# Optimization experiments

Measured on AMD Instinct MI355X. Metric: run time of the kernel, lower is better.

Reference implementation:

```python
import jax, jax.numpy as jnp
import numpy as np

N_HEAD = 16
NEG_BIG = 1e10  # matches the torch module's -10000000000.0 additive mask


def setup_inputs() -> dict:
    key = jax.random.key(0)
    k1, k2, k3 = jax.random.split(key, 3)
    B, T, D = 2, 2048, 1024
    x = jax.random.normal(k1, (B, T, D), dtype=jnp.float32)
    W_attn = jax.random.normal(k2, (D, 3 * D), dtype=jnp.float32) * 0.02
    b_attn = jnp.zeros((3 * D,), dtype=jnp.float32)
    W_proj = jax.random.normal(k3, (D, D), dtype=jnp.float32) * 0.02
    b_proj = jnp.zeros((D,), dtype=jnp.float32)
    return {"x": x, "W_attn": W_attn, "b_attn": b_attn,
            "W_proj": W_proj, "b_proj": b_proj}


def reference(x, W_attn, b_attn, W_proj, b_proj):
    B, T, D = x.shape
    H = N_HEAD
    dh = D // H
    # c_attn: fused qkv projection
    qkv = x @ W_attn + b_attn                      # [B, T, 3D]
    q, k, v = jnp.split(qkv, 3, axis=-1)
    # split heads -> [B, H, T, dh]
    q = q.reshape(B, T, H, dh).transpose(0, 2, 1, 3)
    k = k.reshape(B, T, H, dh).transpose(0, 2, 1, 3)
    v = v.reshape(B, T, H, dh).transpose(0, 2, 1, 3)
    # scores [B, H, T, T]
    w = jnp.einsum("bhqd,bhkd->bhqk", q, k)
    w = w / jnp.sqrt(jnp.float32(dh))              # scale=True
    # causal additive mask: w*b - 1e10*(1-b), b = lower-triangular ones
    bias = jnp.tril(jnp.ones((T, T), dtype=w.dtype))
    w = w * bias - NEG_BIG * (1.0 - bias)
    w = jax.nn.softmax(w, axis=-1)
    a = jnp.einsum("bhqk,bhkd->bhqd", w, v)        # [B, H, T, dh]
    # merge heads
    a = a.transpose(0, 2, 1, 3).reshape(B, T, D)
    # c_proj
    return a @ W_proj + b_proj
```

## Files before the change

kernel.cpp:

```cpp
#include <hip/hip_runtime.h>
#include <hip/hip_bf16.h>


typedef unsigned short u16;
typedef unsigned int u32;
typedef __attribute__((ext_vector_type(4))) float f32x4;
typedef __attribute__((ext_vector_type(16))) float f32x16;
typedef __attribute__((ext_vector_type(8))) short bf16x8;
typedef __attribute__((ext_vector_type(4))) int i32x4;

__device__ __forceinline__ u16 f2bf(float f) {
  unsigned u = __builtin_bit_cast(unsigned, f);
  u += 0x7FFFu + ((u >> 16) & 1u);
  return (u16)(u >> 16);
}

__device__ __forceinline__ u32 cvtpk(float lo, float hi) {
  u32 r;
  asm("v_cvt_pk_bf16_f32 %0, %1, %2" : "=v"(r) : "v"(lo), "v"(hi));
  return r;
}

__device__ __forceinline__ void gl_lds16(const u16* g, u16* l) {
  __builtin_amdgcn_global_load_lds(
      (const __attribute__((address_space(1))) void*)g,
      (__attribute__((address_space(3))) void*)l, 16, 0, 0);
}

__global__ __launch_bounds__(256) void cast_bf16_kernel(const float* __restrict__ in,
                                                        u16* __restrict__ out, int n4) {
  int i = blockIdx.x * 256 + threadIdx.x;
  if (i < n4) {
    float4 f = reinterpret_cast<const float4*>(in)[i];
    ushort4 o;
    o.x = f2bf(f.x); o.y = f2bf(f.y); o.z = f2bf(f.z); o.w = f2bf(f.w);
    reinterpret_cast<ushort4*>(out)[i] = o;
  }
}

__global__ __launch_bounds__(256) void transpose_cast(const float* __restrict__ in,
                                                      u16* __restrict__ out, int R, int C) {
  __shared__ float tile[32][33];
  const int c0 = blockIdx.x * 32, r0 = blockIdx.y * 32;
  const int tx = threadIdx.x, ty = threadIdx.y;
#pragma unroll
  for (int i = 0; i < 4; ++i)
    tile[ty + 8 * i][tx] = in[(size_t)(r0 + ty + 8 * i) * C + c0 + tx];
  __syncthreads();
#pragma unroll
  for (int i = 0; i < 4; ++i)
    out[(size_t)(c0 + ty + 8 * i) * R + r0 + tx] = f2bf(tile[tx][ty + 8 * i]);
}

__global__ __launch_bounds__(256) void gemm_qkv(
    const u16* __restrict__ A, const u16* __restrict__ Bt, const float* __restrict__ bias,
    u16* __restrict__ Qh, u16* __restrict__ Kh, u16* __restrict__ Vh, int K) {
  __shared__ u16 As[128 * 32];
  __shared__ u16 Bs[128 * 32];
  const int tid = threadIdx.x;
  const int wave = tid >> 6, lane = tid & 63;
  const int kg = lane >> 4, rr = lane & 15;
  const int wm = wave >> 1, wn = wave & 1;
  const int nwg = gridDim.x * gridDim.y;
  const int lin = blockIdx.y * gridDim.x + blockIdx.x;
  const int swz = (lin & 7) * (nwg >> 3) + (lin >> 3);
  const int bx = swz % gridDim.x, by = swz / gridDim.x;
  const int rowA0 = by * 128, colB0 = bx * 128;

  const f32x4 z4 = {0.f, 0.f, 0.f, 0.f};
  f32x4 acc[4][4];
#pragma unroll
  for (int i = 0; i < 4; ++i)
#pragma unroll
    for (int j = 0; j < 4; ++j) acc[i][j] = z4;

  const int r_st = tid >> 2;
  const int c_st = (tid & 3) * 8;

  for (int k0 = 0; k0 < K; k0 += 32) {
#pragma unroll
    for (int i = 0; i < 2; ++i) {
      gl_lds16(A + (size_t)(rowA0 + i * 64 + r_st) * K + k0 + c_st,
               As + (i * 256 + (wave << 6)) * 8);
      gl_lds16(Bt + (size_t)(colB0 + i * 64 + r_st) * K + k0 + c_st,
               Bs + (i * 256 + (wave << 6)) * 8);
    }
    __syncthreads();

    bf16x8 af[4], bfr[4];
#pragma unroll
    for (int mi = 0; mi < 4; ++mi)
      af[mi] = *reinterpret_cast<const bf16x8*>(&As[(wm * 64 + mi * 16 + rr) * 32 + kg * 8]);
#pragma unroll
    for (int ni = 0; ni < 4; ++ni)
      bfr[ni] = *reinterpret_cast<const bf16x8*>(&Bs[(wn * 64 + ni * 16 + rr) * 32 + kg * 8]);
#pragma unroll
    for (int mi = 0; mi < 4; ++mi)
#pragma unroll
      for (int ni = 0; ni < 4; ++ni)
        acc[mi][ni] = __builtin_amdgcn_mfma_f32_16x16x32_bf16(af[mi], bfr[ni], acc[mi][ni], 0, 0, 0);
    __syncthreads();
  }

  const float QS = 0.125f * 1.44269504088896f;
#pragma unroll
  for (int mi = 0; mi < 4; ++mi) {
#pragma unroll
    for (int ni = 0; ni < 4; ++ni) {
      const int col = colB0 + wn * 64 + ni * 16 + rr;
      const float bcol = bias[col];
      f32x4 a = acc[mi][ni];
#pragma unroll
      for (int v = 0; v < 4; ++v) {
        const int row = rowA0 + wm * 64 + mi * 16 + kg * 4 + v;
        const float val = a[v] + bcol;
        const int b = row >> 11, t = row & 2047;
        const int which = col >> 10, d = col & 1023;
        const int h = d >> 6, dd = d & 63;
        const size_t idx = (((size_t)(b * 16 + h)) * 2048 + t) * 64 + dd;
        if (which == 0)
          Qh[idx] = f2bf(val * QS);
        else if (which == 1)
          Kh[idx] = f2bf(val);
        else
          Vh[idx] = f2bf(val);
      }
    }
  }
}

__global__ __launch_bounds__(256) void gemm_proj(
    const u16* __restrict__ A, const u16* __restrict__ Bt, const float* __restrict__ bias,
    float* __restrict__ outF, int N, int K) {
  __shared__ u16 As[128 * 32];
  __shared__ u16 Bs[64 * 32];
  const int tid = threadIdx.x;
  const int wave = tid >> 6, lane = tid & 63;
  const int kg = lane >> 4, rr = lane & 15;
  const int nwg = gridDim.x * gridDim.y;
  const int lin = blockIdx.y * gridDim.x + blockIdx.x;
  const int swz = (lin & 7) * (nwg >> 3) + (lin >> 3);
  const int bx = swz % gridDim.x, by = swz / gridDim.x;
  const int rowA0 = by * 128, colB0 = bx * 64;

  const f32x4 z4 = {0.f, 0.f, 0.f, 0.f};
  f32x4 acc[2][4];
#pragma unroll
  for (int i = 0; i < 2; ++i)
#pragma unroll
    for (int j = 0; j < 4; ++j) acc[i][j] = z4;

  const int r_st = tid >> 2;
  const int c_st = (tid & 3) * 8;

  for (int k0 = 0; k0 < K; k0 += 32) {
#pragma unroll
    for (int i = 0; i < 2; ++i)
      gl_lds16(A + (size_t)(rowA0 + i * 64 + r_st) * K + k0 + c_st,
               As + (i * 256 + (wave << 6)) * 8);
    gl_lds16(Bt + (size_t)(colB0 + r_st) * K + k0 + c_st, Bs + (wave << 6) * 8);
    __syncthreads();

    bf16x8 af[2], bfr[4];
#pragma unroll
    for (int mi = 0; mi < 2; ++mi)
      af[mi] = *reinterpret_cast<const bf16x8*>(&As[(wave * 32 + mi * 16 + rr) * 32 + kg * 8]);
#pragma unroll
    for (int ni = 0; ni < 4; ++ni)
      bfr[ni] = *reinterpret_cast<const bf16x8*>(&Bs[(ni * 16 + rr) * 32 + kg * 8]);
#pragma unroll
    for (int mi = 0; mi < 2; ++mi)
#pragma unroll
      for (int ni = 0; ni < 4; ++ni)
        acc[mi][ni] = __builtin_amdgcn_mfma_f32_16x16x32_bf16(af[mi], bfr[ni], acc[mi][ni], 0, 0, 0);
    __syncthreads();
  }

#pragma unroll
  for (int mi = 0; mi < 2; ++mi) {
#pragma unroll
    for (int ni = 0; ni < 4; ++ni) {
      const int col = colB0 + ni * 16 + rr;
      const float bcol = bias[col];
      f32x4 a = acc[mi][ni];
#pragma unroll
      for (int v = 0; v < 4; ++v) {
        const int row = rowA0 + wave * 32 + mi * 16 + kg * 4 + v;
        outF[(size_t)row * N + col] = a[v] + bcol;
      }
    }
  }
}

__global__ __launch_bounds__(256) void transpose_v(const u16* __restrict__ Vh,
                                                   u16* __restrict__ VhT) {
  __shared__ u16 tile[64][72];
  const int tid = threadIdx.x;
  const int t0 = blockIdx.x * 64;
  const int bh = blockIdx.y;
  const u16* src = Vh + ((size_t)bh * 2048 + t0) * 64;
  {
    const int ty = tid >> 2, tx = (tid & 3) * 16;
    *reinterpret_cast<bf16x8*>(&tile[ty][tx]) =
        *reinterpret_cast<const bf16x8*>(src + ty * 64 + tx);
    *reinterpret_cast<bf16x8*>(&tile[ty][tx + 8]) =
        *reinterpret_cast<const bf16x8*>(src + ty * 64 + tx + 8);
  }
  __syncthreads();
  {
    const int dd = tid >> 2, toff = (tid & 3) * 16;
    bf16x8 v0, v1;
#pragma unroll
    for (int j = 0; j < 8; ++j) v0[j] = (short)tile[toff + j][dd];
#pragma unroll
    for (int j = 0; j < 8; ++j) v1[j] = (short)tile[toff + 8 + j][dd];
    u16* dst = VhT + ((size_t)bh * 64 + dd) * 2048 + t0 + toff;
    *reinterpret_cast<bf16x8*>(dst) = v0;
    *reinterpret_cast<bf16x8*>(dst + 8) = v1;
  }
}

__device__ __forceinline__ void load_k(const u16* kptr, bf16x8 (&kA)[4], bf16x8 (&kB)[4]) {
#pragma unroll
  for (int ks = 0; ks < 4; ++ks) {
    kA[ks] = *reinterpret_cast<const bf16x8*>(kptr + ks * 16);
    kB[ks] = *reinterpret_cast<const bf16x8*>(kptr + 2048 + ks * 16);
  }
}

__device__ __forceinline__ void attn_step(
    int kvb, int n64, int myq, int hi, const u16* vbase,
    const bf16x8 (&qf)[4], const bf16x8 (&kA)[4], const bf16x8 (&kB)[4],
    f32x16& oA, f32x16& oB, float& m, float& l) {
  bf16x8 vfA[4], vfB[4];
  const u16* vp = vbase + kvb * 64;
#pragma unroll
  for (int ks = 0; ks < 4; ++ks) {
    vfA[ks] = *reinterpret_cast<const bf16x8*>(vp + ks * 16);
    vfB[ks] = *reinterpret_cast<const bf16x8*>(vp + 32 * 2048 + ks * 16);
  }

  f32x16 sA, sB;
#pragma unroll
  for (int i = 0; i < 16; ++i) { sA[i] = 0.f; sB[i] = 0.f; }
  __builtin_amdgcn_s_setprio(1);
#pragma unroll
  for (int ks = 0; ks < 4; ++ks)
    sA = __builtin_amdgcn_mfma_f32_32x32x16_bf16(kA[ks], qf[ks], sA, 0, 0, 0);
#pragma unroll
  for (int ks = 0; ks < 4; ++ks)
    sB = __builtin_amdgcn_mfma_f32_32x32x16_bf16(kB[ks], qf[ks], sB, 0, 0, 0);
  __builtin_amdgcn_s_setprio(0);

  if (kvb == n64 - 1) {
    const int kv0 = kvb * 64;
#pragma unroll
    for (int r = 0; r < 16; ++r) {
      const int kvA = kv0 + (r & 3) + 8 * (r >> 2) + 4 * hi;
      if (kvA > myq) sA[r] = -1e30f;
      if (kvA + 32 > myq) sB[r] = -1e30f;
    }
  }

  float pmax = -1e30f;
#pragma unroll
  for (int r = 0; r < 16; ++r) pmax = fmaxf(pmax, fmaxf(sA[r], sB[r]));
  pmax = fmaxf(pmax, __shfl_xor(pmax, 32));
  if (!__all(pmax - m <= 8.0f)) {
    const float mn = fmaxf(m, pmax);
    const float sc = __builtin_amdgcn_exp2f(m - mn);
    l *= sc;
    oA *= sc;
    oB *= sc;
    m = mn;
  }
  float rsum = 0.f;
#pragma unroll
  for (int r = 0; r < 16; ++r) {
    const float pa = __builtin_amdgcn_exp2f(sA[r] - m);
    const float pb = __builtin_amdgcn_exp2f(sB[r] - m);
    sA[r] = pa; sB[r] = pb;
    rsum += pa + pb;
  }
  rsum += __shfl_xor(rsum, 32);
  l += rsum;

  u32 pkA[8], pkB[8];
#pragma unroll
  for (int i = 0; i < 8; ++i) {
    pkA[i] = cvtpk(sA[2 * i], sA[2 * i + 1]);
    pkB[i] = cvtpk(sB[2 * i], sB[2 * i + 1]);
  }
  bf16x8 pf[4];
  {
    auto w0 = __builtin_amdgcn_permlane32_swap(pkA[0], pkA[2], false, false);
    auto w1 = __builtin_amdgcn_permlane32_swap(pkA[1], pkA[3], false, false);
    i32x4 t0 = {(int)w0[0], (int)w1[0], (int)w0[1], (int)w1[1]};
    pf[0] = __builtin_bit_cast(bf16x8, t0);
    auto w2 = __builtin_amdgcn_permlane32_swap(pkA[4], pkA[6], false, false);
    auto w3 = __builtin_amdgcn_permlane32_swap(pkA[5], pkA[7], false, false);
    i32x4 t1 = {(int)w2[0], (int)w3[0], (int)w2[1], (int)w3[1]};
    pf[1] = __builtin_bit_cast(bf16x8, t1);
    auto w4 = __builtin_amdgcn_permlane32_swap(pkB[0], pkB[2], false, false);
    auto w5 = __builtin_amdgcn_permlane32_swap(pkB[1], pkB[3], false, false);
    i32x4 t2 = {(int)w4[0], (int)w5[0], (int)w4[1], (int)w5[1]};
    pf[2] = __builtin_bit_cast(bf16x8, t2);
    auto w6 = __builtin_amdgcn_permlane32_swap(pkB[4], pkB[6], false, false);
    auto w7 = __builtin_amdgcn_permlane32_swap(pkB[5], pkB[7], false, false);
    i32x4 t3 = {(int)w6[0], (int)w7[0], (int)w6[1], (int)w7[1]};
    pf[3] = __builtin_bit_cast(bf16x8, t3);
  }

  __builtin_amdgcn_s_setprio(1);
#pragma unroll
  for (int ks = 0; ks < 4; ++ks)
    oA = __builtin_amdgcn_mfma_f32_32x32x16_bf16(vfA[ks], pf[ks], oA, 0, 0, 0);
#pragma unroll
  for (int ks = 0; ks < 4; ++ks)
    oB = __builtin_amdgcn_mfma_f32_32x32x16_bf16(vfB[ks], pf[ks], oB, 0, 0, 0);
  __builtin_amdgcn_s_setprio(0);
}

__global__ __launch_bounds__(256, 2) void attn_fwd(const u16* __restrict__ Qh,
                                                   const u16* __restrict__ Kh,
                                                   const u16* __restrict__ VhT,
                                                   u16* __restrict__ Ab) {
  __shared__ u16 Olq[4][32][80];
  __shared__ float Ml[4][2][32];
  const int tid = threadIdx.x;
  const int wave = tid >> 6, lane = tid & 63;
  const int lq = lane & 31, hi = lane >> 5;
  const int blk = blockIdx.x;
  const int qi = blk >> 5;
  const int bh = blk & 31;
  const int qtile = 63 - qi;
  const int q0 = qtile * 32;
  const int myq = q0 + lq;
  const size_t kvbase = (size_t)bh * 2048;

  const int n64 = (q0 + 32 + 63) >> 6;
  const int base = n64 >> 2, rem = n64 & 3;
  const int cnt = base + (wave < rem ? 1 : 0);
  const int start = wave * base + (wave < rem ? wave : rem);
  const int end = start + cnt;

  bf16x8 qf[4];
  {
    const u16* qptr = Qh + (kvbase + q0 + lq) * 64 + hi * 8;
#pragma unroll
    for (int ks = 0; ks < 4; ++ks)
      qf[ks] = *reinterpret_cast<const bf16x8*>(qptr + ks * 16);
  }

  f32x16 oA, oB;
#pragma unroll
  for (int i = 0; i < 16; ++i) { oA[i] = 0.f; oB[i] = 0.f; }
  float m = -1e30f, l = 0.f;

  const u16* kbase = Kh + (kvbase + lq) * 64 + hi * 8;
  const u16* vbase = VhT + ((size_t)bh * 64 + lq) * 2048 + hi * 8;

  bf16x8 kA0[4], kB0[4], kA1[4], kB1[4];
  int kvb = start;
  if (kvb < end) {
    load_k(kbase + (size_t)kvb * 4096, kA0, kB0);
    while (true) {
      if (kvb + 1 < end) load_k(kbase + (size_t)(kvb + 1) * 4096, kA1, kB1);
      attn_step(kvb, n64, myq, hi, vbase, qf, kA0, kB0, oA, oB, m, l);
      if (++kvb >= end) break;
      if (kvb + 1 < end) load_k(kbase + (size_t)(kvb + 1) * 4096, kA0, kB0);
      attn_step(kvb, n64, myq, hi, vbase, qf, kA1, kB1, oA, oB, m, l);
      if (++kvb >= end) break;
    }
  }

  if (hi == 0) {
    Ml[wave][0][lq] = m;
    Ml[wave][1][lq] = l;
  }
  {
    u32* orow = reinterpret_cast<u32*>(&Olq[wave][lq][0]);
#pragma unroll
    for (int qd = 0; qd < 4; ++qd) {
      const int dh0 = 8 * qd + 4 * hi;
      orow[(dh0 >> 1) + 0] = cvtpk(oA[4 * qd + 0], oA[4 * qd + 1]);
      orow[(dh0 >> 1) + 1] = cvtpk(oA[4 * qd + 2], oA[4 * qd + 3]);
      orow[((dh0 + 32) >> 1) + 0] = cvtpk(oB[4 * qd + 0], oB[4 * qd + 1]);
      orow[((dh0 + 32) >> 1) + 1] = cvtpk(oB[4 * qd + 2], oB[4 * qd + 3]);
    }
  }
  __syncthreads();

  const int col = tid >> 3;
  const int dh0 = (tid & 7) * 8;
  float M = -1e30f;
  float mw[4];
#pragma unroll
  for (int w = 0; w < 4; ++w) { mw[w] = Ml[w][0][col]; M = fmaxf(M, mw[w]); }
  float lsum = 0.f;
  float scw[4];
#pragma unroll
  for (int w = 0; w < 4; ++w) {
    scw[w] = __builtin_amdgcn_exp2f(mw[w] - M);
    lsum += scw[w] * Ml[w][1][col];
  }
  const float inv = 1.0f / lsum;
  float acc8[8];
#pragma unroll
  for (int i = 0; i < 8; ++i) acc8[i] = 0.f;
#pragma unroll
  for (int w = 0; w < 4; ++w) {
    bf16x8 ov = *reinterpret_cast<const bf16x8*>(&Olq[w][col][dh0]);
#pragma unroll
    for (int i = 0; i < 8; ++i) {
      const float f = __builtin_bit_cast(float, ((u32)(u16)ov[i]) << 16);
      acc8[i] += scw[w] * f;
    }
  }
  const int b = bh >> 4, h = bh & 15;
  bf16x8 outv;
#pragma unroll
  for (int i = 0; i < 8; ++i) outv[i] = (short)f2bf(acc8[i] * inv);
  *reinterpret_cast<bf16x8*>(Ab + ((size_t)b * 2048 + q0 + col) * 1024 + h * 64 + dh0) = outv;
}

extern "C" void kernel_launch(void* const* d_in, const int* in_sizes, int n_in,
                              void* d_out, int out_size, void* d_ws, size_t ws_size,
                              hipStream_t stream) {
  const float* x      = (const float*)d_in[0];
  const float* W_attn = (const float*)d_in[1];
  const float* b_attn = (const float*)d_in[2];
  const float* W_proj = (const float*)d_in[3];
  const float* b_proj = (const float*)d_in[4];
  float* out = (float*)d_out;

  u16* xb  = (u16*)d_ws;
  u16* Wat = xb + (size_t)4096 * 1024;
  u16* Wpt = Wat + (size_t)3072 * 1024;
  u16* Qh  = Wpt + (size_t)1024 * 1024;
  u16* Kh  = Qh + (size_t)4194304;
  u16* VhT = Kh + (size_t)4194304;
  u16* Ab  = VhT + (size_t)4194304;
  u16* Vh  = Ab;

  cast_bf16_kernel<<<4096, 256, 0, stream>>>(x, xb, 4096 * 1024 / 4);
  transpose_cast<<<dim3(96, 32), dim3(32, 8), 0, stream>>>(W_attn, Wat, 1024, 3072);
  transpose_cast<<<dim3(32, 32), dim3(32, 8), 0, stream>>>(W_proj, Wpt, 1024, 1024);
  gemm_qkv<<<dim3(24, 32), 256, 0, stream>>>(xb, Wat, b_attn, Qh, Kh, Vh, 1024);
  transpose_v<<<dim3(32, 32), 256, 0, stream>>>(Vh, VhT);
  attn_fwd<<<dim3(2048), 256, 0, stream>>>(Qh, Kh, VhT, Ab);
  gemm_proj<<<dim3(16, 32), 256, 0, stream>>>(Ab, Wpt, b_proj, out, 1024, 1024);
}
```

Measured before the change: 218.2 us.

## Merge prep kernels, write V transposed from QKV GEMM, use permlane reductions

Merges the x cast and both weight transpose-casts into one launch, cutting launch count. The QKV GEMM epilogue now writes V directly in transposed layout, which removes the separate transpose_v kernel and its extra round trip through memory. In attention, the cross-half max and sum reductions use permlane32_swap instead of shfl_xor, and the LDS output staging pad shrinks from 80 to 72. The transposed V stores from the GEMM epilogue are strided scalar 2-byte writes, so they may coalesce poorly.

Result: faster. 213.5 us (-2.1%).

```diff
diff --git a/kernel.cpp b/kernel.cpp
--- a/kernel.cpp
+++ b/kernel.cpp
@@ -21,28 +21,47 @@
   return r;
 }
 
+__device__ __forceinline__ void xc32(float x, float& y0, float& y1) {
+  u32 xu = __builtin_bit_cast(u32, x);
+  auto sw = __builtin_amdgcn_permlane32_swap(xu, xu, false, false);
+  y0 = __builtin_bit_cast(float, (u32)sw[0]);
+  y1 = __builtin_bit_cast(float, (u32)sw[1]);
+}
+
 __device__ __forceinline__ void gl_lds16(const u16* g, u16* l) {
   __builtin_amdgcn_global_load_lds(
       (const __attribute__((address_space(1))) void*)g,
       (__attribute__((address_space(3))) void*)l, 16, 0, 0);
 }
 
-__global__ __launch_bounds__(256) void cast_bf16_kernel(const float* __restrict__ in,
-                                                        u16* __restrict__ out, int n4) {
-  int i = blockIdx.x * 256 + threadIdx.x;
-  if (i < n4) {
-    float4 f = reinterpret_cast<const float4*>(in)[i];
+__global__ __launch_bounds__(256) void prep(const float* __restrict__ x, u16* __restrict__ xb,
+                                            const float* __restrict__ Wa, u16* __restrict__ Wat,
+                                            const float* __restrict__ Wp, u16* __restrict__ Wpt) {
+  __shared__ float tile[32][33];
+  const int blk = blockIdx.x;
+  const int tid = threadIdx.x;
+  if (blk < 4096) {
+    const int i = blk * 256 + tid;
+    float4 f = reinterpret_cast<const float4*>(x)[i];
     ushort4 o;
     o.x = f2bf(f.x); o.y = f2bf(f.y); o.z = f2bf(f.z); o.w = f2bf(f.w);
-    reinterpret_cast<ushort4*>(out)[i] = o;
-  }
-}
-
-__global__ __launch_bounds__(256) void transpose_cast(const float* __restrict__ in,
-                                                      u16* __restrict__ out, int R, int C) {
-  __shared__ float tile[32][33];
-  const int c0 = blockIdx.x * 32, r0 = blockIdx.y * 32;
-  const int tx = threadIdx.x, ty = threadIdx.y;
+    reinterpret_cast<ushort4*>(xb)[i] = o;
+    return;
+  }
+  const float* in;
+  u16* out;
+  int R, C, bx, by;
+  if (blk < 4096 + 3072) {
+    const int bb = blk - 4096;
+    in = Wa; out = Wat; R = 1024; C = 3072;
+    bx = bb % 96; by = bb / 96;
+  } else {
+    const int bb = blk - 7168;
+    in = Wp; out = Wpt; R = 1024; C = 1024;
+    bx = bb % 32; by = bb / 32;
+  }
+  const int c0 = bx * 32, r0 = by * 32;
+  const int tx = tid & 31, ty = tid >> 5;
 #pragma unroll
   for (int i = 0; i < 4; ++i)
     tile[ty + 8 * i][tx] = in[(size_t)(r0 + ty + 8 * i) * C + c0 + tx];
@@ -54,7 +73,7 @@
 
 __global__ __launch_bounds__(256) void gemm_qkv(
     const u16* __restrict__ A, const u16* __restrict__ Bt, const float* __restrict__ bias,
-    u16* __restrict__ Qh, u16* __restrict__ Kh, u16* __restrict__ Vh, int K) {
+    u16* __restrict__ Qh, u16* __restrict__ Kh, u16* __restrict__ VhT, int K) {
   __shared__ u16 As[128 * 32];
   __shared__ u16 Bs[128 * 32];
   const int tid = threadIdx.x;
@@ -117,13 +136,13 @@
         const int b = row >> 11, t = row & 2047;
         const int which = col >> 10, d = col & 1023;
         const int h = d >> 6, dd = d & 63;
-        const size_t idx = (((size_t)(b * 16 + h)) * 2048 + t) * 64 + dd;
+        const size_t bh = (size_t)(b * 16 + h);
         if (which == 0)
-          Qh[idx] = f2bf(val * QS);
+          Qh[(bh * 2048 + t) * 64 + dd] = f2bf(val * QS);
         else if (which == 1)
-          Kh[idx] = f2bf(val);
+          Kh[(bh * 2048 + t) * 64 + dd] = f2bf(val);
         else
-          Vh[idx] = f2bf(val);
+          VhT[(bh * 64 + dd) * 2048 + t] = f2bf(val);
       }
     }
   }
@@ -192,34 +211,6 @@
   }
 }
 
-__global__ __launch_bounds__(256) void transpose_v(const u16* __restrict__ Vh,
-                                                   u16* __restrict__ VhT) {
-  __shared__ u16 tile[64][72];
-  const int tid = threadIdx.x;
-  const int t0 = blockIdx.x * 64;
-  const int bh = blockIdx.y;
-  const u16* src = Vh + ((size_t)bh * 2048 + t0) * 64;
-  {
-    const int ty = tid >> 2, tx = (tid & 3) * 16;
-    *reinterpret_cast<bf16x8*>(&tile[ty][tx]) =
-        *reinterpret_cast<const bf16x8*>(src + ty * 64 + tx);
-    *reinterpret_cast<bf16x8*>(&tile[ty][tx + 8]) =
-        *reinterpret_cast<const bf16x8*>(src + ty * 64 + tx + 8);
-  }
-  __syncthreads();
-  {
-    const int dd = tid >> 2, toff = (tid & 3) * 16;
-    bf16x8 v0, v1;
-#pragma unroll
-    for (int j = 0; j < 8; ++j) v0[j] = (short)tile[toff + j][dd];
-#pragma unroll
-    for (int j = 0; j < 8; ++j) v1[j] = (short)tile[toff + 8 + j][dd];
-    u16* dst = VhT + ((size_t)bh * 64 + dd) * 2048 + t0 + toff;
-    *reinterpret_cast<bf16x8*>(dst) = v0;
-    *reinterpret_cast<bf16x8*>(dst + 8) = v1;
-  }
-}
-
 __device__ __forceinline__ void load_k(const u16* kptr, bf16x8 (&kA)[4], bf16x8 (&kB)[4]) {
 #pragma unroll
   for (int ks = 0; ks < 4; ++ks) {
@@ -265,7 +256,11 @@
   float pmax = -1e30f;
 #pragma unroll
   for (int r = 0; r < 16; ++r) pmax = fmaxf(pmax, fmaxf(sA[r], sB[r]));
-  pmax = fmaxf(pmax, __shfl_xor(pmax, 32));
+  {
+    float y0, y1;
+    xc32(pmax, y0, y1);
+    pmax = fmaxf(y0, y1);
+  }
   if (!__all(pmax - m <= 8.0f)) {
     const float mn = fmaxf(m, pmax);
     const float sc = __builtin_amdgcn_exp2f(m - mn);
@@ -282,7 +277,11 @@
     sA[r] = pa; sB[r] = pb;
     rsum += pa + pb;
   }
-  rsum += __shfl_xor(rsum, 32);
+  {
+    float y0, y1;
+    xc32(rsum, y0, y1);
+    rsum = y0 + y1;
+  }
   l += rsum;
 
   u32 pkA[8], pkB[8];
@@ -325,7 +324,7 @@
                                                    const u16* __restrict__ Kh,
                                                    const u16* __restrict__ VhT,
                                                    u16* __restrict__ Ab) {
-  __shared__ u16 Olq[4][32][80];
+  __shared__ u16 Olq[4][32][72];
   __shared__ float Ml[4][2][32];
   const int tid = threadIdx.x;
   const int wave = tid >> 6, lane = tid & 63;
@@ -441,13 +440,9 @@
   u16* Kh  = Qh + (size_t)4194304;
   u16* VhT = Kh + (size_t)4194304;
   u16* Ab  = VhT + (size_t)4194304;
-  u16* Vh  = Ab;
-
-  cast_bf16_kernel<<<4096, 256, 0, stream>>>(x, xb, 4096 * 1024 / 4);
-  transpose_cast<<<dim3(96, 32), dim3(32, 8), 0, stream>>>(W_attn, Wat, 1024, 3072);
-  transpose_cast<<<dim3(32, 32), dim3(32, 8), 0, stream>>>(W_proj, Wpt, 1024, 1024);
-  gemm_qkv<<<dim3(24, 32), 256, 0, stream>>>(xb, Wat, b_attn, Qh, Kh, Vh, 1024);
-  transpose_v<<<dim3(32, 32), 256, 0, stream>>>(Vh, VhT);
+
+  prep<<<8192, 256, 0, stream>>>(x, xb, W_attn, Wat, W_proj, Wpt);
+  gemm_qkv<<<dim3(24, 32), 256, 0, stream>>>(xb, Wat, b_attn, Qh, Kh, VhT, 1024);
   attn_fwd<<<dim3(2048), 256, 0, stream>>>(Qh, Kh, VhT, Ab);
   gemm_proj<<<dim3(16, 32), 256, 0, stream>>>(Ab, Wpt, b_proj, out, 1024, 1024);
 }
```
